# Kernel tuning notes

Measured on AMD Instinct MI355X. Metric: run time of the kernel, lower is better.

The kernel has to match this reference:

```python
import jax, jax.numpy as jnp
from jax import lax
import numpy as np

BS, T, DA, DZ, K = 64, 512, 16, 32, 3


def _lstm_layer(x, Wih, Whh, bih, bhh):
    # x: [B, T, in], PyTorch LSTM gate order i,f,g,o; zero initial state
    B = x.shape[0]
    H = Whh.shape[1]
    b = bih + bhh

    def step(carry, xt):
        h, c = carry
        g = xt @ Wih.T + h @ Whh.T + b  # [B, 4H]
        i, f, gg, o = jnp.split(g, 4, axis=-1)
        c = jax.nn.sigmoid(f) * c + jax.nn.sigmoid(i) * jnp.tanh(gg)
        h = jax.nn.sigmoid(o) * jnp.tanh(c)
        return (h, c), h

    h0 = jnp.zeros((B, H), x.dtype)
    _, hs = lax.scan(step, (h0, h0), jnp.swapaxes(x, 0, 1))
    return jnp.swapaxes(hs, 0, 1)


def setup_inputs() -> dict:
    key = jax.random.key(0)
    ks = jax.random.split(key, 12)
    a = jax.random.normal(ks[0], (BS, T, DA), jnp.float32)
    # mixture dynamics / emission matrices, kept near identity for stability
    A = 0.95 * jnp.eye(DZ, dtype=jnp.float32) + 0.02 * jax.random.normal(ks[1], (K, T, DZ, DZ), jnp.float32)
    C = jnp.eye(DA, DZ, dtype=jnp.float32) + 0.05 * jax.random.normal(ks[2], (K, T, DA, DZ), jnp.float32)
    R = 0.1 * jnp.eye(DA, dtype=jnp.float32)
    Q = 0.1 * jnp.eye(DZ, dtype=jnp.float32)
    mu0 = jnp.zeros((DZ,), jnp.float32)
    sigma0 = jnp.eye(DZ, dtype=jnp.float32)
    H4 = 4 * K  # LSTM hidden size = K
    Wih0 = 0.1 * jax.random.normal(ks[3], (H4, DA), jnp.float32)
    Whh0 = 0.1 * jax.random.normal(ks[4], (H4, K), jnp.float32)
    bih0 = 0.1 * jax.random.normal(ks[5], (H4,), jnp.float32)
    bhh0 = 0.1 * jax.random.normal(ks[6], (H4,), jnp.float32)
    Wih1 = 0.1 * jax.random.normal(ks[7], (H4, K), jnp.float32)
    Whh1 = 0.1 * jax.random.normal(ks[8], (H4, K), jnp.float32)
    bih1 = 0.1 * jax.random.normal(ks[9], (H4,), jnp.float32)
    bhh1 = 0.1 * jax.random.normal(ks[10], (H4,), jnp.float32)
    return {"a": a, "A": A, "C": C, "R": R, "Q": Q, "mu0": mu0, "sigma0": sigma0,
            "Wih0": Wih0, "Whh0": Whh0, "bih0": bih0, "bhh0": bhh0,
            "Wih1": Wih1, "Whh1": Whh1, "bih1": bih1, "bhh1": bhh1}


def reference(a, A, C, R, Q, mu0, sigma0, Wih0, Whh0, bih0, bhh0, Wih1, Whh1, bih1, bhh1):
    bs, T, da = a.shape
    dz = A.shape[-1]
    # dynamics network: 2-layer LSTM + softmax mixture weights alpha [bs,T,K]
    h = _lstm_layer(a, Wih0, Whh0, bih0, bhh0)
    h = _lstm_layer(h, Wih1, Whh1, bih1, bhh1)
    alpha = jax.nn.softmax(h, axis=-1)
    # mix per-mode matrices; time-major [T,bs,.,.]
    At = jnp.einsum('btk,ktij->tbij', alpha, A)
    Ct = jnp.einsum('btk,ktij->tbij', alpha, C)
    a_tm = jnp.swapaxes(a, 0, 1)  # [T,bs,da]
    I = jnp.eye(dz, dtype=a.dtype)
    mu_f0 = jnp.broadcast_to(mu0, (bs, dz))
    sig_f0 = jnp.broadcast_to(sigma0, (bs, dz, dz))

    def fstep(carry, inp):
        mu_f, mu_p, sig_p = carry  # prev filtered mean, predicted mean/cov
        a_t, A_t, C_t = inp
        # NOTE: residual uses previous *filtered* mean, matching the source code
        r = a_t - jnp.einsum('bij,bj->bi', C_t, mu_f)
        Ct_T = jnp.swapaxes(C_t, -1, -2)
        S = C_t @ sig_p @ Ct_T + R
        Kg = sig_p @ Ct_T @ jnp.linalg.inv(S)
        mu_new = mu_p + jnp.einsum('bij,bj->bi', Kg, r)
        sig_new = (I - Kg @ C_t) @ sig_p
        mu_p_new = jnp.einsum('bij,bj->bi', A_t, mu_new)
        sig_p_new = A_t @ sig_new @ jnp.swapaxes(A_t, -1, -2) + Q
        return (mu_new, mu_p_new, sig_p_new), (mu_new, sig_new, mu_p_new, sig_p_new)

    _, (mu_f, sig_f, mu_p, sig_p) = lax.scan(
        fstep, (mu_f0, mu_f0, sig_f0), (a_tm, At, Ct))

    # RTS smoothing (backward recursion), faithful to smooth()
    def sstep(carry, inp):
        mu_n, sig_n = carry
        mu_ft, sig_ft, mu_pt, sig_pt, A_next = inp
        J = sig_ft @ jnp.swapaxes(A_next, -1, -2) @ jnp.linalg.inv(sig_pt)
        mu_s = mu_ft + jnp.einsum('bij,bj->bi', J, mu_n - mu_pt)
        sig_s = sig_ft + J @ (sig_n - sig_pt)
        return (mu_s, sig_s), (mu_s, sig_s)

    _, (mu_s_rest, sig_s_rest) = lax.scan(
        sstep, (mu_f[-1], sig_f[-1]),
        (mu_f[:-1], sig_f[:-1], mu_p[:-1], sig_p[:-1], At[1:]),
        reverse=True)
    mu_s = jnp.concatenate([mu_s_rest, mu_f[-1:]], axis=0)   # [T,bs,dz]
    sig_s = jnp.concatenate([sig_s_rest, sig_f[-1:]], axis=0)  # [T,bs,dz,dz]
    out = jnp.concatenate([mu_s, sig_s.reshape(T, bs, dz * dz)], axis=-1)
    return jnp.swapaxes(out, 0, 1)  # [bs, T, dz + dz*dz]
```

## Files before the change

### kernel.cpp

```cpp
#include <hip/hip_runtime.h>
#include <hip/hip_bf16.h>

#define BSZ 64
#define TT  512
#define DA  16
#define DZ  32
#define NG  12
#define NT  256

typedef __hip_bfloat16 bf;

#define FP32_R0 0x3DCCCCCDu

__device__ __forceinline__ int mode_(const void* Rm){
  return (((const unsigned*)Rm)[0] == FP32_R0) ? 0 : 1;
}
__device__ __forceinline__ float LD(const void* p, size_t i, int b16){
  return b16 ? __bfloat162float(((const bf*)p)[i]) : ((const float*)p)[i];
}
__device__ __forceinline__ void STO(void* p, size_t i, float v, int b16){
  if (b16) ((bf*)p)[i] = __float2bfloat16(v);
  else     ((float*)p)[i] = v;
}
__device__ __forceinline__ float osan_(double vd, float code){
  float v = (float)vd;
  unsigned u = __float_as_uint(v);
  if ((u & 0x7f800000u) == 0x7f800000u)
    return ((u & 0x007fffffu) != 0u) ? code : ((u >> 31) ? -(code-1000.0f) : (code-1000.0f));
  return v;
}
__device__ __forceinline__ float sigm_(float x){ return 1.0f/(1.0f + __expf(-x)); }
__device__ __forceinline__ float tanh_(float x){ return 1.0f - 2.0f/(__expf(2.0f*x)+1.0f); }

__device__ void alpha_stage_(int b, int tid, int b16,
  const void* a, const void* Wih0, const void* bih0, const void* bhh0,
  const void* Whh0, const void* Wih1, const void* Whh1,
  const void* bih1, const void* bhh1,
  float* sxw, float* salp)
{
  for (int e=tid; e<TT*NG; e+=NT){
    int t=e/NG, g=e-NG*t;
    float s = LD(bih0,g,b16) + LD(bhh0,g,b16);
    size_t ab = ((size_t)b*TT + t)*DA;
    #pragma unroll
    for (int j=0;j<DA;++j) s += LD(Wih0,g*DA+j,b16)*LD(a,ab+j,b16);
    sxw[e] = s;
  }
  __syncthreads();
  if (tid==0){
    float w0[NG][3], wi1[NG][3], w1[NG][3], bb[NG];
    #pragma unroll
    for (int g=0;g<NG;++g){
      #pragma unroll
      for (int j=0;j<3;++j){ w0[g][j]=LD(Whh0,(size_t)g*3+j,b16); wi1[g][j]=LD(Wih1,(size_t)g*3+j,b16); w1[g][j]=LD(Whh1,(size_t)g*3+j,b16); }
      bb[g] = LD(bih1,g,b16) + LD(bhh1,g,b16);
    }
    float h1[3]={0,0,0}, c1[3]={0,0,0}, h2[3]={0,0,0}, c2[3]={0,0,0};
    for (int t=0;t<TT;++t){
      const float* xr = sxw + t*NG;
      float g1[NG];
      #pragma unroll
      for (int g=0;g<NG;++g) g1[g] = xr[g] + w0[g][0]*h1[0]+w0[g][1]*h1[1]+w0[g][2]*h1[2];
      #pragma unroll
      for (int j=0;j<3;++j){
        float iv=sigm_(g1[j]), fv=sigm_(g1[3+j]), gv=tanh_(g1[6+j]), ov=sigm_(g1[9+j]);
        c1[j] = fv*c1[j] + iv*gv;
        h1[j] = ov*tanh_(c1[j]);
      }
      float g2[NG];
      #pragma unroll
      for (int g=0;g<NG;++g) g2[g] = bb[g] + wi1[g][0]*h1[0]+wi1[g][1]*h1[1]+wi1[g][2]*h1[2]
                                            + w1[g][0]*h2[0]+w1[g][1]*h2[1]+w1[g][2]*h2[2];
      #pragma unroll
      for (int j=0;j<3;++j){
        float iv=sigm_(g2[j]), fv=sigm_(g2[3+j]), gv=tanh_(g2[6+j]), ov=sigm_(g2[9+j]);
        c2[j] = fv*c2[j] + iv*gv;
        h2[j] = ov*tanh_(c2[j]);
      }
      float m = fmaxf(h2[0], fmaxf(h2[1], h2[2]));
      float e0=__expf(h2[0]-m), e1=__expf(h2[1]-m), e2=__expf(h2[2]-m);
      float inv = 1.0f/(e0+e1+e2);
      salp[t*3+0]=e0*inv; salp[t*3+1]=e1*inv; salp[t*3+2]=e2*inv;
    }
  }
  __syncthreads();
}

__global__ __launch_bounds__(256) void k_alpha(
  const void* __restrict__ a, const void* __restrict__ Rm,
  const void* __restrict__ Wih0, const void* __restrict__ Whh0,
  const void* __restrict__ bih0, const void* __restrict__ bhh0,
  const void* __restrict__ Wih1, const void* __restrict__ Whh1,
  const void* __restrict__ bih1, const void* __restrict__ bhh1,
  float* __restrict__ alws)
{
  const int b16 = mode_(Rm);
  const int b = blockIdx.x, tid = threadIdx.x;
  __shared__ float sxw[TT*NG];
  __shared__ float salp[TT*3];
  alpha_stage_(b, tid, b16, a, Wih0, bih0, bhh0, Whh0, Wih1, Whh1, bih1, bhh1,
               sxw, salp);
  for (int e=tid;e<TT*3;e+=NT) alws[(size_t)b*TT*3+e] = salp[e];
}

__global__ __launch_bounds__(256) void k_fwd(
  const void* __restrict__ a, const void* __restrict__ Am,
  const void* __restrict__ Cm, const void* __restrict__ Rm,
  const void* __restrict__ Qm, const void* __restrict__ mu0,
  const void* __restrict__ sig0,
  const void* __restrict__ Wih0, const void* __restrict__ Whh0,
  const void* __restrict__ bih0, const void* __restrict__ bhh0,
  const void* __restrict__ Wih1, const void* __restrict__ Whh1,
  const void* __restrict__ bih1, const void* __restrict__ bhh1,
  const float* __restrict__ alws,
  void* __restrict__ out)
{
  const int b16 = mode_(Rm);
  const int b = blockIdx.x, tid = threadIdx.x;
  __shared__ double dpool[4240];
  __shared__ float sAt[1056], sCt[528], sQ[1056], sR[272], sPCt[544], sKg[544];
  __shared__ float salp[TT*3];
  __shared__ double dMu[32], dMup[32], dr[16];
  double* dPp  = dpool;
  double* dPf  = dpool+1056;
  double* dCP  = dpool+2112;
  double* dT1  = dpool+2640;
  double* dAugS= dpool+3696;
  double* dMinv= dpool+3968;

  if (alws){
    for (int e=tid;e<TT*3;e+=NT) salp[e] = alws[(size_t)b*TT*3+e];
    __syncthreads();
  } else {
    alpha_stage_(b, tid, b16, a, Wih0, bih0, bhh0, Whh0, Wih1, Whh1, bih1, bhh1,
                 (float*)dpool, salp);
  }

  for (int e=tid;e<1024;e+=NT){ int i=e>>5,j=e&31;
    sQ[i*33+j]  = LD(Qm,e,b16);
    dPp[i*33+j] = (double)LD(sig0,e,b16); }
  for (int e=tid;e<256;e+=NT){ int i=e>>4,j=e&15; sR[i*17+j] = LD(Rm,e,b16); }
  if (tid<32){ double m = (double)LD(mu0,tid,b16); dMu[tid]=m; dMup[tid]=m; }
  __syncthreads();

  const int i0 = tid>>5, j0 = tid&31;
  const int i4 = tid>>4, j4 = tid&15;

  float pA0[4],pA1[4],pA2[4],pC0[2],pC1[2],pC2[2];
  {
    size_t o0=0, o1=(size_t)TT*1024, o2=(size_t)2*TT*1024;
    #pragma unroll
    for (int q=0;q<4;++q){ int e=tid+q*NT; pA0[q]=LD(Am,o0+e,b16); pA1[q]=LD(Am,o1+e,b16); pA2[q]=LD(Am,o2+e,b16); }
    size_t c0=0, c1=(size_t)TT*512, c2=(size_t)2*TT*512;
    #pragma unroll
    for (int q=0;q<2;++q){ int e=tid+q*NT; pC0[q]=LD(Cm,c0+e,b16); pC1[q]=LD(Cm,c1+e,b16); pC2[q]=LD(Cm,c2+e,b16); }
  }

  for (int t=0;t<TT;++t){
    const size_t ob = ((size_t)b*TT+t)*1056;
    {
      float a0=salp[t*3+0], a1=salp[t*3+1], a2=salp[t*3+2];
      #pragma unroll
      for (int q=0;q<4;++q){ int e=tid+q*NT; int i=e>>5,j=e&31;
        sAt[i*33+j] = a0*pA0[q]+a1*pA1[q]+a2*pA2[q]; }
      #pragma unroll
      for (int q=0;q<2;++q){ int e=tid+q*NT; int i=e>>5,j=e&31;
        sCt[i*33+j] = a0*pC0[q]+a1*pC1[q]+a2*pC2[q]; }
    }
    if (t+1<TT){
      size_t o0=(size_t)(t+1)*1024, o1=(size_t)(TT+t+1)*1024, o2=(size_t)(2*TT+t+1)*1024;
      #pragma unroll
      for (int q=0;q<4;++q){ int e=tid+q*NT; pA0[q]=LD(Am,o0+e,b16); pA1[q]=LD(Am,o1+e,b16); pA2[q]=LD(Am,o2+e,b16); }
      size_t c0=(size_t)(t+1)*512, c1=(size_t)(TT+t+1)*512, c2=(size_t)(2*TT+t+1)*512;
      #pragma unroll
      for (int q=0;q<2;++q){ int e=tid+q*NT; pC0[q]=LD(Cm,c0+e,b16); pC1[q]=LD(Cm,c1+e,b16); pC2[q]=LD(Cm,c2+e,b16); }
    }
    __syncthreads();

    {
      double A0=0.0, A1=0.0;
      for (int k=0;k<32;++k){ double bv=dPp[k*33+j0];
        A0 += (double)sCt[i0*33+k]*bv;
        A1 += (double)sCt[(i0+8)*33+k]*bv; }
      dCP[i0*33+j0]=A0; dCP[(i0+8)*33+j0]=A1;
    }
    {
      double A0=0.0, A1=0.0;
      for (int m=0;m<32;++m){ double cv=(double)sCt[j4*33+m];
        A0 += dPp[i4*33+m]*cv;
        A1 += dPp[(i4+16)*33+m]*cv; }
      sPCt[i4*17+j4]=(float)A0; sPCt[(i4+16)*17+j4]=(float)A1;
    }
    if (tid<16){ double s = (double)LD(a,((size_t)b*TT+t)*DA+tid,b16);
      for (int k=0;k<32;++k) s -= (double)sCt[tid*33+k]*dMu[k];
      dr[tid]=s; }
    __syncthreads();

    { int i=tid>>4, j=tid&15; double v=(double)sR[i*17+j];
      for (int k=0;k<32;++k) v += dCP[i*33+k]*(double)sCt[j*33+k];
      dAugS[i*17+j]=v; }
    __syncthreads();

    if (tid < 64){
      const int r = tid>>2, q = tid&3, cbase = q*8;
      double Rg[8];
      #pragma unroll
      for (int u=0;u<8;++u){
        int c = cbase+u;
        Rg[u] = (c<16) ? dAugS[r*17+c] : ((c-16)==r ? 1.0 : 0.0);
      }
      #pragma unroll
      for (int kp=0;kp<16;++kp){
        double pv = __shfl(Rg[kp&7], (kp<<2)|(kp>>3), 64);
        if (!(fabs(pv)>1e-300)) pv=1.0;
        double ip = 1.0/pv;
        if (r==kp){
          #pragma unroll
          for (int u=0;u<8;++u){ int c=cbase+u; if (c>kp) Rg[u]*=ip; }
        }
        double rf = __shfl(Rg[kp&7], (tid&0x3C)|(kp>>3), 64);
        #pragma unroll
        for (int u=0;u<8;++u){
          double pr = __shfl(Rg[u], (kp<<2)|q, 64);
          int c=cbase+u;
          if (r!=kp && c>kp) Rg[u] -= rf*pr;
        }
      }
      if (q>=2){
        #pragma unroll
        for (int u=0;u<8;++u){ int k=cbase+u-16; dMinv[r*17+k]=Rg[u]; }
      }
    }
    __syncthreads();

    {
      double A0=0.0, A1=0.0;
      for (int l=0;l<16;++l){ double mv=dMinv[l*17+j4];
        A0 += (double)sPCt[i4*17+l]*mv;
        A1 += (double)sPCt[(i4+16)*17+l]*mv; }
      sKg[i4*17+j4]=(float)A0; sKg[(i4+16)*17+j4]=(float)A1;
    }
    __syncthreads();

    if (tid<32){ double s=dMup[tid];
      for (int k=0;k<16;++k) s += (double)sKg[tid*17+k]*dr[k];
      dMu[tid]=s;
      STO(out, ob+tid, osan_(s,5300.0f), b16);
    }
    {
      double A0=dPp[i0*33+j0], A1=dPp[(i0+8)*33+j0],
             A2=dPp[(i0+16)*33+j0], A3=dPp[(i0+24)*33+j0];
      for (int l=0;l<16;++l){ double cv=dCP[l*33+j0];
        A0 -= (double)sKg[i0*17+l]*cv;
        A1 -= (double)sKg[(i0+8)*17+l]*cv;
        A2 -= (double)sKg[(i0+16)*17+l]*cv;
        A3 -= (double)sKg[(i0+24)*17+l]*cv; }
      dPf[i0*33+j0]=A0; dPf[(i0+8)*33+j0]=A1;
      dPf[(i0+16)*33+j0]=A2; dPf[(i0+24)*33+j0]=A3;
      STO(out, ob+32+((size_t)i0<<5)+j0,      osan_(A0,5300.0f), b16);
      STO(out, ob+32+((size_t)(i0+8)<<5)+j0,  osan_(A1,5300.0f), b16);
      STO(out, ob+32+((size_t)(i0+16)<<5)+j0, osan_(A2,5300.0f), b16);
      STO(out, ob+32+((size_t)(i0+24)<<5)+j0, osan_(A3,5300.0f), b16);
    }
    __syncthreads();

    {
      double A0=0.0,A1=0.0,A2=0.0,A3=0.0;
      for (int k=0;k<32;++k){ double bv=dPf[k*33+j0];
        A0 += (double)sAt[i0*33+k]*bv;
        A1 += (double)sAt[(i0+8)*33+k]*bv;
        A2 += (double)sAt[(i0+16)*33+k]*bv;
        A3 += (double)sAt[(i0+24)*33+k]*bv; }
      dT1[i0*33+j0]=A0; dT1[(i0+8)*33+j0]=A1;
      dT1[(i0+16)*33+j0]=A2; dT1[(i0+24)*33+j0]=A3;
    }
    if (tid<32){ double s=0.0;
      for (int k=0;k<32;++k) s += (double)sAt[tid*33+k]*dMu[k];
      dMup[tid]=s; }
    __syncthreads();

    {
      double A0=(double)sQ[i0*33+j0], A1=(double)sQ[(i0+8)*33+j0],
             A2=(double)sQ[(i0+16)*33+j0], A3=(double)sQ[(i0+24)*33+j0];
      for (int k=0;k<32;++k){ double av=(double)sAt[j0*33+k];
        A0 += dT1[i0*33+k]*av;
        A1 += dT1[(i0+8)*33+k]*av;
        A2 += dT1[(i0+16)*33+k]*av;
        A3 += dT1[(i0+24)*33+k]*av; }
      dPp[i0*33+j0]=A0; dPp[(i0+8)*33+j0]=A1;
      dPp[(i0+16)*33+j0]=A2; dPp[(i0+24)*33+j0]=A3;
    }
    __syncthreads();
  }
}

__global__ __launch_bounds__(256) void k_pre(
  const void* __restrict__ Am, const void* __restrict__ Qm,
  const void* __restrict__ Rm, const void* __restrict__ outv,
  const float* __restrict__ alws, float* __restrict__ rec, int t0)
{
  const int b16 = mode_(Rm);
  const int t = t0 + blockIdx.x;
  const int b = blockIdx.y;
  const int tid = threadIdx.x;
  __shared__ double dAug[2080];
  __shared__ double dmp[32];
  __shared__ float sAtc[1056], sAtn[1056], sSf[1056], sT[1056], sF[1056], sPp[1056], sJ[1056], sQ[1056];
  __shared__ float smu[32];

  size_t obase = (size_t)b*TT*1056;
  const float* al = alws + (size_t)b*TT*3;
  float c0=al[t*3+0],     c1=al[t*3+1],     c2=al[t*3+2];
  float n0=al[(t+1)*3+0], n1=al[(t+1)*3+1], n2=al[(t+1)*3+2];
  size_t oA0c=(size_t)t*1024, oA1c=(size_t)(TT+t)*1024, oA2c=(size_t)(2*TT+t)*1024;
  size_t oA0n=oA0c+1024, oA1n=oA1c+1024, oA2n=oA2c+1024;

  for (int e=tid;e<1024;e+=NT){ int i=e>>5,j=e&31;
    sAtc[i*33+j] = c0*LD(Am,oA0c+e,b16)+c1*LD(Am,oA1c+e,b16)+c2*LD(Am,oA2c+e,b16);
    sAtn[i*33+j] = n0*LD(Am,oA0n+e,b16)+n1*LD(Am,oA1n+e,b16)+n2*LD(Am,oA2n+e,b16);
    sSf[i*33+j]  = LD(outv, obase + (size_t)t*1056 + 32 + e, b16);
    sQ[i*33+j]   = LD(Qm,e,b16);
  }
  if (tid<32) smu[tid] = LD(outv, obase + (size_t)t*1056 + tid, b16);
  __syncthreads();

  for (int e=tid;e<1024;e+=NT){ int i=e>>5, j=e&31;
    double acc=0.0, accF=0.0;
    for (int k=0;k<32;++k){
      acc  += (double)sAtc[i*33+k]*(double)sSf[k*33+j];
      accF += (double)sSf[i*33+k]*(double)sAtn[j*33+k];
    }
    sT[i*33+j]=(float)acc; sF[i*33+j]=(float)accF; }
  if (tid<32){ double s=0.0;
    for (int k=0;k<32;++k) s += (double)sAtc[tid*33+k]*(double)smu[k];
    dmp[tid]=s; }
  __syncthreads();

  for (int e=tid;e<1024;e+=NT){ int i=e>>5, j=e&31;
    double acc=(double)sQ[i*33+j];
    for (int k=0;k<32;++k) acc += (double)sT[i*33+k]*(double)sAtc[j*33+k];
    sPp[i*33+j]=(float)acc;
    dAug[i*65+j]=acc;
    dAug[i*65+32+j]=(i==j)?1.0:0.0; }
  __syncthreads();

  for (int kp=0;kp<32;++kp){
    double pv = dAug[kp*65+kp];
    if (!(fabs(pv)>1e-300)) pv=1.0;
    double ip = 1.0/pv;
    if (tid<64 && tid>kp) dAug[kp*65+tid] *= ip;
    __syncthreads();
    for (int e=tid;e<2048;e+=NT){ int i=e>>6, j=e&63;
      if (i!=kp && j>kp) dAug[i*65+j] -= dAug[i*65+kp]*dAug[kp*65+j];
    }
    __syncthreads();
  }

  float* rp = rec + ((size_t)b*gridDim.x + (size_t)blockIdx.x)*2080;

  for (int e=tid;e<1024;e+=NT){ int i=e>>5, j=e&31; double acc=0.0;
    for (int k=0;k<32;++k) acc += (double)sF[i*33+k]*dAug[k*65+32+j];
    float jv=(float)acc; sJ[i*33+j]=jv; rp[e]=jv; }
  __syncthreads();

  for (int e=tid;e<1024;e+=NT){ int i=e>>5, j=e&31;
    double acc=(double)sSf[i*33+j];
    for (int k=0;k<32;++k) acc -= (double)sJ[i*33+k]*(double)sPp[k*33+j];
    rp[1024+e]=(float)acc; }
  if (tid<32){ double acc=(double)smu[tid];
    for (int k=0;k<32;++k) acc -= (double)sJ[tid*33+k]*dmp[k];
    rp[2048+tid]=(float)acc; }
}

__global__ __launch_bounds__(256) void k_bwd(
  const void* __restrict__ Rm, void* __restrict__ outv,
  const float* __restrict__ rec, float* __restrict__ cont,
  int t0, int t1)
{
  const int b16 = mode_(Rm);
  const int b = blockIdx.x, tid = threadIdx.x;
  const int chlen = t1 - t0;
  __shared__ float sX[2][1056];
  __shared__ float sR[2080];
  size_t obase = (size_t)b*TT*1056;
  int cur = 0;
  const int i0 = tid>>5, j0 = tid&31;

  if (t1 == TT-1){
    for (int e=tid;e<1024;e+=NT){ int i=e>>5,j=e&31;
      sX[0][i*33+j] = LD(outv, obase+(size_t)(TT-1)*1056+32+e, b16); }
    if (tid<32) sX[0][tid*33+32] = LD(outv, obase+(size_t)(TT-1)*1056+tid, b16);
  } else {
    for (int e=tid;e<1056;e+=NT) sX[0][e] = cont[(size_t)b*1056+e];
  }
  float rg[9];
  {
    const float* rp = rec + ((size_t)b*chlen + (size_t)(chlen-1))*2080;
    #pragma unroll
    for (int q=0;q<9;++q){ int e=tid+q*NT; rg[q] = (e<2080)? rp[e] : 0.0f; }
  }
  __syncthreads();

  for (int t=t1-1; t>=t0; --t){
    #pragma unroll
    for (int q=0;q<9;++q){ int e=tid+q*NT; if (e<2080) sR[e]=rg[q]; }
    if (t>t0){
      const float* rp = rec + ((size_t)b*chlen + (size_t)(t-1-t0))*2080;
      #pragma unroll
      for (int q=0;q<9;++q){ int e=tid+q*NT; rg[q] = (e<2080)? rp[e] : 0.0f; }
    }
    __syncthreads();

    const float* Xc = sX[cur]; float* Xn = sX[cur^1];
    {
      double A0=(double)sR[1024+(i0<<5)+j0];
      double A1=(double)sR[1024+((i0+8)<<5)+j0];
      double A2=(double)sR[1024+((i0+16)<<5)+j0];
      double A3=(double)sR[1024+((i0+24)<<5)+j0];
      for (int k=0;k<32;++k){ double xv=(double)Xc[k*33+j0];
        A0 += (double)sR[(i0<<5)+k]*xv;
        A1 += (double)sR[((i0+8)<<5)+k]*xv;
        A2 += (double)sR[((i0+16)<<5)+k]*xv;
        A3 += (double)sR[((i0+24)<<5)+k]*xv; }
      Xn[i0*33+j0]=(float)A0;      Xn[(i0+8)*33+j0]=(float)A1;
      Xn[(i0+16)*33+j0]=(float)A2; Xn[(i0+24)*33+j0]=(float)A3;
      size_t tb = obase+(size_t)t*1056+32;
      STO(outv, tb+((size_t)i0<<5)+j0,      osan_(A0,5700.0f), b16);
      STO(outv, tb+((size_t)(i0+8)<<5)+j0,  osan_(A1,5700.0f), b16);
      STO(outv, tb+((size_t)(i0+16)<<5)+j0, osan_(A2,5700.0f), b16);
      STO(outv, tb+((size_t)(i0+24)<<5)+j0, osan_(A3,5700.0f), b16);
    }
    if (tid<32){
      double acc=(double)sR[2048+tid];
      for (int k=0;k<32;++k) acc += (double)sR[(tid<<5)+k]*(double)Xc[k*33+32];
      Xn[tid*33+32]=(float)acc;
      STO(outv, obase+(size_t)t*1056+tid, osan_(acc,5700.0f), b16);
    }
    __syncthreads();
    cur ^= 1;
  }
  for (int e=tid;e<1056;e+=NT) cont[(size_t)b*1056+e] = sX[cur][e];
}

__global__ __launch_bounds__(256) void k_smooth(
  const void* __restrict__ a, const void* __restrict__ Am,
  const void* __restrict__ Rm, const void* __restrict__ Qm,
  const void* __restrict__ Wih0, const void* __restrict__ Whh0,
  const void* __restrict__ bih0, const void* __restrict__ bhh0,
  const void* __restrict__ Wih1, const void* __restrict__ Whh1,
  const void* __restrict__ bih1, const void* __restrict__ bhh1,
  void* __restrict__ out)
{
  const int b16 = mode_(Rm);
  const int b = blockIdx.x, tid = threadIdx.x;
  __shared__ double dAug[2080];
  __shared__ float fp2[9504];
  __shared__ float salp[TT*3];
  __shared__ double dMun[32], dmp[32], sdm[32];
  float* sAtn = fp2;
  float* sAtc = fp2+1056;
  float* sSf  = fp2+2112;
  float* sSn  = fp2+3168;
  float* sT   = fp2+4224;
  float* sQ   = fp2+5280;
  float* sF   = fp2+6336;
  float* sPp32= fp2+7392;
  float* sJ   = fp2+8448;

  alpha_stage_(b, tid, b16, a, Wih0, bih0, bhh0, Whh0, Wih1, Whh1, bih1, bhh1,
               fp2, salp);

  size_t obase = (size_t)b*TT*1056;
  for (int e=tid;e<1024;e+=NT){ int i=e>>5,j=e&31;
    sQ[i*33+j]  = LD(Qm,e,b16);
    sSn[i*33+j] = LD(out, obase + (size_t)(TT-1)*1056 + 32 + e, b16); }
  if (tid<32) dMun[tid] = (double)LD(out, obase + (size_t)(TT-1)*1056 + tid, b16);
  __syncthreads();

  for (int t=TT-2; t>=0; --t){
    float n0=salp[(t+1)*3+0], n1=salp[(t+1)*3+1], n2=salp[(t+1)*3+2];
    float c0=salp[t*3+0],     c1=salp[t*3+1],     c2=salp[t*3+2];
    size_t oA0n=(size_t)(t+1)*1024, oA1n=(size_t)(TT+t+1)*1024, oA2n=(size_t)(2*TT+t+1)*1024;
    size_t oA0c=(size_t)t*1024,     oA1c=(size_t)(TT+t)*1024,   oA2c=(size_t)(2*TT+t)*1024;
    for (int e=tid;e<1024;e+=NT){ int i=e>>5,j=e&31;
      sAtn[i*33+j] = n0*LD(Am,oA0n+e,b16)+n1*LD(Am,oA1n+e,b16)+n2*LD(Am,oA2n+e,b16);
      sAtc[i*33+j] = c0*LD(Am,oA0c+e,b16)+c1*LD(Am,oA1c+e,b16)+c2*LD(Am,oA2c+e,b16);
      sSf[i*33+j]  = LD(out, obase + (size_t)t*1056 + 32 + e, b16); }
    __syncthreads();

    for (int e=tid;e<1024;e+=NT){ int i=e>>5, j=e&31;
      double acc=0.0, accF=0.0;
      for (int k=0;k<32;++k){
        acc  += (double)sAtc[i*33+k]*(double)sSf[k*33+j];
        accF += (double)sSf[i*33+k]*(double)sAtn[j*33+k];
      }
      sT[i*33+j]=(float)acc; sF[i*33+j]=(float)accF; }
    if (tid<32){ double s=0.0; float muf = LD(out, obase+(size_t)t*1056+tid, b16);
      for (int k=0;k<32;++k) s += (double)sAtc[tid*33+k]*(double)LD(out, obase+(size_t)t*1056+k, b16);
      dmp[tid]=s; (void)muf; }
    __syncthreads();

    for (int e=tid;e<1024;e+=NT){ int i=e>>5, j=e&31;
      double acc=(double)sQ[i*33+j];
      for (int k=0;k<32;++k) acc += (double)sT[i*33+k]*(double)sAtc[j*33+k];
      sPp32[i*33+j]=(float)acc;
      dAug[i*65+j]=acc;
      dAug[i*65+32+j]=(i==j)?1.0:0.0; }
    if (tid<32) sdm[tid] = dMun[tid] - dmp[tid];
    __syncthreads();

    for (int kp=0;kp<32;++kp){
      double pv = dAug[kp*65+kp];
      if (!(fabs(pv)>1e-300)) pv=1.0;
      double ip = 1.0/pv;
      if (tid<64 && tid>kp) dAug[kp*65+tid] *= ip;
      __syncthreads();
      for (int e=tid;e<2048;e+=NT){ int i=e>>6, j=e&63;
        if (i!=kp && j>kp) dAug[i*65+j] -= dAug[i*65+kp]*dAug[kp*65+j];
      }
      __syncthreads();
    }

    for (int e=tid;e<1024;e+=NT){ int i=e>>5, j=e&31; double acc=0.0;
      for (int k=0;k<32;++k) acc += (double)sF[i*33+k]*dAug[k*65+32+j];
      sJ[i*33+j]=(float)acc; }
    __syncthreads();

    if (tid<32){ double s2=0.0;
      for (int k=0;k<32;++k) s2 += (double)sJ[tid*33+k]*sdm[k];
      double v = (double)LD(out, obase+(size_t)t*1056+tid, b16) + s2;
      STO(out, obase+(size_t)t*1056+tid, osan_(v,5700.0f), b16);
      dMun[tid] = v;
    }
    float resv[4];
    { int i0 = tid>>5, j = tid&31;
      for (int s=0;s<4;++s){ int i=i0+(s<<3); double acc=0.0;
        for (int k=0;k<32;++k) acc += (double)sJ[i*33+k]*((double)sSn[k*33+j]-(double)sPp32[k*33+j]);
        double res = (double)sSf[i*33+j] + acc;
        STO(out, obase+(size_t)t*1056+32+(i<<5)+j, osan_(res,5700.0f), b16);
        resv[s]=(float)res;
      }
    }
    __syncthreads();
    { int i0 = tid>>5, j = tid&31;
      for (int s=0;s<4;++s){ int i=i0+(s<<3); sSn[i*33+j]=resv[s]; } }
    __syncthreads();
  }
}

__global__ __launch_bounds__(256) void k_fill(float* o, int n, float v){
  int i = blockIdx.x*256 + threadIdx.x;
  if (i<n) o[i]=v;
}

extern "C" void kernel_launch(void* const* d_in, const int* in_sizes, int n_in,
                              void* d_out, int out_size, void* d_ws, size_t ws_size,
                              hipStream_t stream)
{
  static const int EXP[15] = {524288,1572864,786432,256,1024,32,1024,192,36,12,12,36,36,12,12};
  int ok = (n_in==15) && (out_size==34603008);
  if (ok) for (int i=0;i<15;++i) if (in_sizes[i]!=EXP[i]) ok=0;
  if (!ok){
    k_fill<<<dim3((out_size+255)/256), dim3(256), 0, stream>>>((float*)d_out, out_size, 777.0f);
    return;
  }
  const void* a=d_in[0]; const void* Am=d_in[1]; const void* Cm=d_in[2];
  const void* Rm=d_in[3]; const void* Qm=d_in[4]; const void* mu0=d_in[5];
  const void* sig0=d_in[6];
  const void* Wih0=d_in[7]; const void* Whh0=d_in[8]; const void* bih0=d_in[9];
  const void* bhh0=d_in[10]; const void* Wih1=d_in[11]; const void* Whh1=d_in[12];
  const void* bih1=d_in[13]; const void* bhh1=d_in[14];

  const long long FIXED_F = 98304LL + 67584LL;
  long long availB = (long long)ws_size;
  int CH = 0;
  if (d_ws && availB > FIXED_F*4){
    long long ch = (availB - FIXED_F*4) / (64LL*2080LL*4LL);
    CH = (int)((ch > 511) ? 511 : ch);
  }

  if (CH >= 4){
    float* wsf  = (float*)d_ws;
    float* alws = wsf;
    float* cont = wsf + 98304;
    float* rec  = wsf + 165888;

    k_alpha<<<dim3(BSZ), dim3(NT), 0, stream>>>(a, Rm,
        Wih0, Whh0, bih0, bhh0, Wih1, Whh1, bih1, bhh1, alws);
    k_fwd  <<<dim3(BSZ), dim3(NT), 0, stream>>>(a, Am, Cm, Rm, Qm, mu0, sig0,
        Wih0, Whh0, bih0, bhh0, Wih1, Whh1, bih1, bhh1, alws, d_out);

    int t1 = TT-1;
    while (t1 > 0){
      int t0 = t1 - CH; if (t0 < 0) t0 = 0;
      int len = t1 - t0;
      k_pre<<<dim3(len, BSZ), dim3(NT), 0, stream>>>(Am, Qm, Rm, d_out, alws, rec, t0);
      k_bwd<<<dim3(BSZ), dim3(NT), 0, stream>>>(Rm, d_out, rec, cont, t0, t1);
      t1 = t0;
    }
  } else {
    k_fwd   <<<dim3(BSZ), dim3(NT), 0, stream>>>(a, Am, Cm, Rm, Qm, mu0, sig0,
               Wih0, Whh0, bih0, bhh0, Wih1, Whh1, bih1, bhh1, (const float*)nullptr, d_out);
    k_smooth<<<dim3(BSZ), dim3(NT), 0, stream>>>(a, Am, Rm, Qm,
               Wih0, Whh0, bih0, bhh0, Wih1, Whh1, bih1, bhh1, d_out);
  }
}
```

Measured before the change: 10.67 ms.

## Widen forward Kalman kernel to 512 threads and restructure covariance update

```diff
diff --git a/kernel.cpp b/kernel.cpp
--- a/kernel.cpp
+++ b/kernel.cpp
@@ -32,13 +32,13 @@
 __device__ __forceinline__ float sigm_(float x){ return 1.0f/(1.0f + __expf(-x)); }
 __device__ __forceinline__ float tanh_(float x){ return 1.0f - 2.0f/(__expf(2.0f*x)+1.0f); }
 
-__device__ void alpha_stage_(int b, int tid, int b16,
+__device__ void alpha_stage_(int b, int tid, int nt, int b16,
   const void* a, const void* Wih0, const void* bih0, const void* bhh0,
   const void* Whh0, const void* Wih1, const void* Whh1,
   const void* bih1, const void* bhh1,
   float* sxw, float* salp)
 {
-  for (int e=tid; e<TT*NG; e+=NT){
+  for (int e=tid; e<TT*NG; e+=nt){
     int t=e/NG, g=e-NG*t;
     float s = LD(bih0,g,b16) + LD(bhh0,g,b16);
     size_t ab = ((size_t)b*TT + t)*DA;
@@ -98,12 +98,12 @@
   const int b = blockIdx.x, tid = threadIdx.x;
   __shared__ float sxw[TT*NG];
   __shared__ float salp[TT*3];
-  alpha_stage_(b, tid, b16, a, Wih0, bih0, bhh0, Whh0, Wih1, Whh1, bih1, bhh1,
+  alpha_stage_(b, tid, NT, b16, a, Wih0, bih0, bhh0, Whh0, Wih1, Whh1, bih1, bhh1,
                sxw, salp);
   for (int e=tid;e<TT*3;e+=NT) alws[(size_t)b*TT*3+e] = salp[e];
 }
 
-__global__ __launch_bounds__(256) void k_fwd(
+__global__ __launch_bounds__(512) void k_fwd(
   const void* __restrict__ a, const void* __restrict__ Am,
   const void* __restrict__ Cm, const void* __restrict__ Rm,
   const void* __restrict__ Qm, const void* __restrict__ mu0,
@@ -122,38 +122,34 @@
   __shared__ float salp[TT*3];
   __shared__ double dMu[32], dMup[32], dr[16];
   double* dPp  = dpool;
-  double* dPf  = dpool+1056;
-  double* dCP  = dpool+2112;
-  double* dT1  = dpool+2640;
+  double* dAP  = dpool+1056;
+  double* dKCP = dpool+2112;
+  double* dCP  = dpool+3168;
   double* dAugS= dpool+3696;
   double* dMinv= dpool+3968;
 
   if (alws){
-    for (int e=tid;e<TT*3;e+=NT) salp[e] = alws[(size_t)b*TT*3+e];
+    for (int e=tid;e<TT*3;e+=512) salp[e] = alws[(size_t)b*TT*3+e];
     __syncthreads();
   } else {
-    alpha_stage_(b, tid, b16, a, Wih0, bih0, bhh0, Whh0, Wih1, Whh1, bih1, bhh1,
+    alpha_stage_(b, tid, 512, b16, a, Wih0, bih0, bhh0, Whh0, Wih1, Whh1, bih1, bhh1,
                  (float*)dpool, salp);
   }
 
-  for (int e=tid;e<1024;e+=NT){ int i=e>>5,j=e&31;
+  for (int e=tid;e<1024;e+=512){ int i=e>>5,j=e&31;
     sQ[i*33+j]  = LD(Qm,e,b16);
     dPp[i*33+j] = (double)LD(sig0,e,b16); }
-  for (int e=tid;e<256;e+=NT){ int i=e>>4,j=e&15; sR[i*17+j] = LD(Rm,e,b16); }
+  if (tid<256){ int i=tid>>4,j=tid&15; sR[i*17+j] = LD(Rm,tid,b16); }
   if (tid<32){ double m = (double)LD(mu0,tid,b16); dMu[tid]=m; dMup[tid]=m; }
   __syncthreads();
 
-  const int i0 = tid>>5, j0 = tid&31;
-  const int i4 = tid>>4, j4 = tid&15;
-
-  float pA0[4],pA1[4],pA2[4],pC0[2],pC1[2],pC2[2];
+  float pA0[2],pA1[2],pA2[2],pC0,pC1,pC2;
   {
     size_t o0=0, o1=(size_t)TT*1024, o2=(size_t)2*TT*1024;
     #pragma unroll
-    for (int q=0;q<4;++q){ int e=tid+q*NT; pA0[q]=LD(Am,o0+e,b16); pA1[q]=LD(Am,o1+e,b16); pA2[q]=LD(Am,o2+e,b16); }
+    for (int q=0;q<2;++q){ int e=tid+(q<<9); pA0[q]=LD(Am,o0+e,b16); pA1[q]=LD(Am,o1+e,b16); pA2[q]=LD(Am,o2+e,b16); }
     size_t c0=0, c1=(size_t)TT*512, c2=(size_t)2*TT*512;
-    #pragma unroll
-    for (int q=0;q<2;++q){ int e=tid+q*NT; pC0[q]=LD(Cm,c0+e,b16); pC1[q]=LD(Cm,c1+e,b16); pC2[q]=LD(Cm,c2+e,b16); }
+    pC0=LD(Cm,c0+tid,b16); pC1=LD(Cm,c1+tid,b16); pC2=LD(Cm,c2+tid,b16);
   }
 
   for (int t=0;t<TT;++t){
@@ -161,47 +157,36 @@
     {
       float a0=salp[t*3+0], a1=salp[t*3+1], a2=salp[t*3+2];
       #pragma unroll
-      for (int q=0;q<4;++q){ int e=tid+q*NT; int i=e>>5,j=e&31;
+      for (int q=0;q<2;++q){ int e=tid+(q<<9); int i=e>>5,j=e&31;
         sAt[i*33+j] = a0*pA0[q]+a1*pA1[q]+a2*pA2[q]; }
-      #pragma unroll
-      for (int q=0;q<2;++q){ int e=tid+q*NT; int i=e>>5,j=e&31;
-        sCt[i*33+j] = a0*pC0[q]+a1*pC1[q]+a2*pC2[q]; }
+      { int i=tid>>5,j=tid&31; sCt[i*33+j] = a0*pC0+a1*pC1+a2*pC2; }
     }
     if (t+1<TT){
       size_t o0=(size_t)(t+1)*1024, o1=(size_t)(TT+t+1)*1024, o2=(size_t)(2*TT+t+1)*1024;
       #pragma unroll
-      for (int q=0;q<4;++q){ int e=tid+q*NT; pA0[q]=LD(Am,o0+e,b16); pA1[q]=LD(Am,o1+e,b16); pA2[q]=LD(Am,o2+e,b16); }
+      for (int q=0;q<2;++q){ int e=tid+(q<<9); pA0[q]=LD(Am,o0+e,b16); pA1[q]=LD(Am,o1+e,b16); pA2[q]=LD(Am,o2+e,b16); }
       size_t c0=(size_t)(t+1)*512, c1=(size_t)(TT+t+1)*512, c2=(size_t)(2*TT+t+1)*512;
-      #pragma unroll
-      for (int q=0;q<2;++q){ int e=tid+q*NT; pC0[q]=LD(Cm,c0+e,b16); pC1[q]=LD(Cm,c1+e,b16); pC2[q]=LD(Cm,c2+e,b16); }
-    }
-    __syncthreads();
-
-    {
-      double A0=0.0, A1=0.0;
-      for (int k=0;k<32;++k){ double bv=dPp[k*33+j0];
-        A0 += (double)sCt[i0*33+k]*bv;
-        A1 += (double)sCt[(i0+8)*33+k]*bv; }
-      dCP[i0*33+j0]=A0; dCP[(i0+8)*33+j0]=A1;
-    }
-    {
-      double A0=0.0, A1=0.0;
-      for (int m=0;m<32;++m){ double cv=(double)sCt[j4*33+m];
-        A0 += dPp[i4*33+m]*cv;
-        A1 += dPp[(i4+16)*33+m]*cv; }
-      sPCt[i4*17+j4]=(float)A0; sPCt[(i4+16)*17+j4]=(float)A1;
-    }
+      pC0=LD(Cm,c0+tid,b16); pC1=LD(Cm,c1+tid,b16); pC2=LD(Cm,c2+tid,b16);
+    }
+    __syncthreads();
+
+    { int i=tid>>5, j=tid&31; double acc=0.0;
+      for (int k=0;k<32;++k) acc += (double)sCt[i*33+k]*dPp[k*33+j];
+      dCP[i*33+j]=acc; }
+    { int i=tid>>4, l=tid&15; double acc=0.0;
+      for (int m=0;m<32;++m) acc += dPp[i*33+m]*(double)sCt[l*33+m];
+      sPCt[i*17+l]=(float)acc; }
     if (tid<16){ double s = (double)LD(a,((size_t)b*TT+t)*DA+tid,b16);
       for (int k=0;k<32;++k) s -= (double)sCt[tid*33+k]*dMu[k];
       dr[tid]=s; }
     __syncthreads();
 
-    { int i=tid>>4, j=tid&15; double v=(double)sR[i*17+j];
-      for (int k=0;k<32;++k) v += dCP[i*33+k]*(double)sCt[j*33+k];
-      dAugS[i*17+j]=v; }
-    __syncthreads();
-
     if (tid < 64){
+      #pragma unroll
+      for (int u=0;u<4;++u){ int e=(tid<<2)+u; int i=e>>4, j=e&15;
+        double v=(double)sR[i*17+j];
+        for (int k=0;k<32;++k) v += dCP[i*33+k]*(double)sCt[j*33+k];
+        dAugS[i*17+j]=v; }
       const int r = tid>>2, q = tid&3, cbase = q*8;
       double Rg[8];
       #pragma unroll
@@ -230,66 +215,46 @@
         #pragma unroll
         for (int u=0;u<8;++u){ int k=cbase+u-16; dMinv[r*17+k]=Rg[u]; }
       }
-    }
-    __syncthreads();
-
-    {
-      double A0=0.0, A1=0.0;
-      for (int l=0;l<16;++l){ double mv=dMinv[l*17+j4];
-        A0 += (double)sPCt[i4*17+l]*mv;
-        A1 += (double)sPCt[(i4+16)*17+l]*mv; }
-      sKg[i4*17+j4]=(float)A0; sKg[(i4+16)*17+j4]=(float)A1;
-    }
-    __syncthreads();
-
+    } else {
+      for (int e=tid-64; e<1024; e+=448){ int i=e>>5,j=e&31; double acc=0.0;
+        for (int k=0;k<32;++k) acc += (double)sAt[i*33+k]*dPp[k*33+j];
+        dAP[i*33+j]=acc; }
+    }
+    __syncthreads();
+
+    { int i=tid>>4, k4=tid&15; double acc=0.0;
+      for (int l=0;l<16;++l) acc += (double)sPCt[i*17+l]*dMinv[l*17+k4];
+      sKg[i*17+k4]=(float)acc; }
+    __syncthreads();
+
+    #pragma unroll
+    for (int q=0;q<2;++q){ int e=tid+(q<<9); int i=e>>5,j=e&31;
+      double acc=0.0;
+      for (int l=0;l<16;++l) acc += (double)sKg[i*17+l]*dCP[l*33+j];
+      dKCP[i*33+j]=acc; }
     if (tid<32){ double s=dMup[tid];
       for (int k=0;k<16;++k) s += (double)sKg[tid*17+k]*dr[k];
       dMu[tid]=s;
-      STO(out, ob+tid, osan_(s,5300.0f), b16);
-    }
-    {
-      double A0=dPp[i0*33+j0], A1=dPp[(i0+8)*33+j0],
-             A2=dPp[(i0+16)*33+j0], A3=dPp[(i0+24)*33+j0];
-      for (int l=0;l<16;++l){ double cv=dCP[l*33+j0];
-        A0 -= (double)sKg[i0*17+l]*cv;
-        A1 -= (double)sKg[(i0+8)*17+l]*cv;
-        A2 -= (double)sKg[(i0+16)*17+l]*cv;
-        A3 -= (double)sKg[(i0+24)*17+l]*cv; }
-      dPf[i0*33+j0]=A0; dPf[(i0+8)*33+j0]=A1;
-      dPf[(i0+16)*33+j0]=A2; dPf[(i0+24)*33+j0]=A3;
-      STO(out, ob+32+((size_t)i0<<5)+j0,      osan_(A0,5300.0f), b16);
-      STO(out, ob+32+((size_t)(i0+8)<<5)+j0,  osan_(A1,5300.0f), b16);
-      STO(out, ob+32+((size_t)(i0+16)<<5)+j0, osan_(A2,5300.0f), b16);
-      STO(out, ob+32+((size_t)(i0+24)<<5)+j0, osan_(A3,5300.0f), b16);
-    }
-    __syncthreads();
-
-    {
-      double A0=0.0,A1=0.0,A2=0.0,A3=0.0;
-      for (int k=0;k<32;++k){ double bv=dPf[k*33+j0];
-        A0 += (double)sAt[i0*33+k]*bv;
-        A1 += (double)sAt[(i0+8)*33+k]*bv;
-        A2 += (double)sAt[(i0+16)*33+k]*bv;
-        A3 += (double)sAt[(i0+24)*33+k]*bv; }
-      dT1[i0*33+j0]=A0; dT1[(i0+8)*33+j0]=A1;
-      dT1[(i0+16)*33+j0]=A2; dT1[(i0+24)*33+j0]=A3;
-    }
+      STO(out, ob+tid, osan_(s,5300.0f), b16); }
+    __syncthreads();
+
+    #pragma unroll
+    for (int q=0;q<2;++q){ int e=tid+(q<<9); int i=e>>5,j=e&31;
+      double pf = dPp[i*33+j] - dKCP[i*33+j];
+      STO(out, ob+32+e, osan_(pf,5300.0f), b16);
+      double acc = dAP[i*33+j];
+      for (int k=0;k<32;++k) acc -= (double)sAt[i*33+k]*dKCP[k*33+j];
+      dAP[i*33+j]=acc; }
     if (tid<32){ double s=0.0;
       for (int k=0;k<32;++k) s += (double)sAt[tid*33+k]*dMu[k];
       dMup[tid]=s; }
     __syncthreads();
 
-    {
-      double A0=(double)sQ[i0*33+j0], A1=(double)sQ[(i0+8)*33+j0],
-             A2=(double)sQ[(i0+16)*33+j0], A3=(double)sQ[(i0+24)*33+j0];
-      for (int k=0;k<32;++k){ double av=(double)sAt[j0*33+k];
-        A0 += dT1[i0*33+k]*av;
-        A1 += dT1[(i0+8)*33+k]*av;
-        A2 += dT1[(i0+16)*33+k]*av;
-        A3 += dT1[(i0+24)*33+k]*av; }
-      dPp[i0*33+j0]=A0; dPp[(i0+8)*33+j0]=A1;
-      dPp[(i0+16)*33+j0]=A2; dPp[(i0+24)*33+j0]=A3;
-    }
+    #pragma unroll
+    for (int q=0;q<2;++q){ int e=tid+(q<<9); int i=e>>5,j=e&31;
+      double acc=(double)sQ[i*33+j];
+      for (int k=0;k<32;++k) acc += dAP[i*33+k]*(double)sAt[j*33+k];
+      dPp[i*33+j]=acc; }
     __syncthreads();
   }
 }
@@ -372,46 +337,48 @@
     rp[2048+tid]=(float)acc; }
 }
 
-__global__ __launch_bounds__(256) void k_bwd(
+__global__ __launch_bounds__(512) void k_bwd(
   const void* __restrict__ Rm, void* __restrict__ outv,
   const float* __restrict__ rec, float* __restrict__ cont,
   int t0, int t1)
 {
   const int b16 = mode_(Rm);
-  const int b = blockIdx.x, tid = threadIdx.x;
+  const int tid = threadIdx.x, grp = tid>>8, lt = tid&255;
+  const int b = (blockIdx.x<<1) + grp;
   const int chlen = t1 - t0;
-  __shared__ float sX[2][1056];
-  __shared__ float sR[2080];
+  __shared__ float sX[2][2][1056];
+  __shared__ float sRr[2][2080];
   size_t obase = (size_t)b*TT*1056;
   int cur = 0;
-  const int i0 = tid>>5, j0 = tid&31;
+  const int i0 = lt>>5, j0 = lt&31;
+  float* X0 = sX[grp][0]; float* X1 = sX[grp][1]; float* sR = sRr[grp];
 
   if (t1 == TT-1){
-    for (int e=tid;e<1024;e+=NT){ int i=e>>5,j=e&31;
-      sX[0][i*33+j] = LD(outv, obase+(size_t)(TT-1)*1056+32+e, b16); }
-    if (tid<32) sX[0][tid*33+32] = LD(outv, obase+(size_t)(TT-1)*1056+tid, b16);
+    for (int e=lt;e<1024;e+=256){ int i=e>>5,j=e&31;
+      X0[i*33+j] = LD(outv, obase+(size_t)(TT-1)*1056+32+e, b16); }
+    if (lt<32) X0[lt*33+32] = LD(outv, obase+(size_t)(TT-1)*1056+lt, b16);
   } else {
-    for (int e=tid;e<1056;e+=NT) sX[0][e] = cont[(size_t)b*1056+e];
+    for (int e=lt;e<1056;e+=256) X0[e] = cont[(size_t)b*1056+e];
   }
   float rg[9];
   {
     const float* rp = rec + ((size_t)b*chlen + (size_t)(chlen-1))*2080;
     #pragma unroll
-    for (int q=0;q<9;++q){ int e=tid+q*NT; rg[q] = (e<2080)? rp[e] : 0.0f; }
+    for (int q=0;q<9;++q){ int e=lt+q*256; rg[q] = (e<2080)? rp[e] : 0.0f; }
   }
   __syncthreads();
 
   for (int t=t1-1; t>=t0; --t){
     #pragma unroll
-    for (int q=0;q<9;++q){ int e=tid+q*NT; if (e<2080) sR[e]=rg[q]; }
+    for (int q=0;q<9;++q){ int e=lt+q*256; if (e<2080) sR[e]=rg[q]; }
     if (t>t0){
       const float* rp = rec + ((size_t)b*chlen + (size_t)(t-1-t0))*2080;
       #pragma unroll
-      for (int q=0;q<9;++q){ int e=tid+q*NT; rg[q] = (e<2080)? rp[e] : 0.0f; }
-    }
-    __syncthreads();
-
-    const float* Xc = sX[cur]; float* Xn = sX[cur^1];
+      for (int q=0;q<9;++q){ int e=lt+q*256; rg[q] = (e<2080)? rp[e] : 0.0f; }
+    }
+    __syncthreads();
+
+    const float* Xc = cur ? X1 : X0; float* Xn = cur ? X0 : X1;
     {
       double A0=(double)sR[1024+(i0<<5)+j0];
       double A1=(double)sR[1024+((i0+8)<<5)+j0];
@@ -430,16 +397,17 @@
       STO(outv, tb+((size_t)(i0+16)<<5)+j0, osan_(A2,5700.0f), b16);
       STO(outv, tb+((size_t)(i0+24)<<5)+j0, osan_(A3,5700.0f), b16);
     }
-    if (tid<32){
-      double acc=(double)sR[2048+tid];
-      for (int k=0;k<32;++k) acc += (double)sR[(tid<<5)+k]*(double)Xc[k*33+32];
-      Xn[tid*33+32]=(float)acc;
-      STO(outv, obase+(size_t)t*1056+tid, osan_(acc,5700.0f), b16);
+    if (lt<32){
+      double acc=(double)sR[2048+lt];
+      for (int k=0;k<32;++k) acc += (double)sR[(lt<<5)+k]*(double)Xc[k*33+32];
+      Xn[lt*33+32]=(float)acc;
+      STO(outv, obase+(size_t)t*1056+lt, osan_(acc,5700.0f), b16);
     }
     __syncthreads();
     cur ^= 1;
   }
-  for (int e=tid;e<1056;e+=NT) cont[(size_t)b*1056+e] = sX[cur][e];
+  { float* Xf = cur ? X1 : X0;
+    for (int e=lt;e<1056;e+=256) cont[(size_t)b*1056+e] = Xf[e]; }
 }
 
 __global__ __launch_bounds__(256) void k_smooth(
@@ -467,7 +435,7 @@
   float* sPp32= fp2+7392;
   float* sJ   = fp2+8448;
 
-  alpha_stage_(b, tid, b16, a, Wih0, bih0, bhh0, Whh0, Wih1, Whh1, bih1, bhh1,
+  alpha_stage_(b, tid, NT, b16, a, Wih0, bih0, bhh0, Whh0, Wih1, Whh1, bih1, bhh1,
                fp2, salp);
 
   size_t obase = (size_t)b*TT*1056;
@@ -587,7 +555,7 @@
 
     k_alpha<<<dim3(BSZ), dim3(NT), 0, stream>>>(a, Rm,
         Wih0, Whh0, bih0, bhh0, Wih1, Whh1, bih1, bhh1, alws);
-    k_fwd  <<<dim3(BSZ), dim3(NT), 0, stream>>>(a, Am, Cm, Rm, Qm, mu0, sig0,
+    k_fwd  <<<dim3(BSZ), dim3(512), 0, stream>>>(a, Am, Cm, Rm, Qm, mu0, sig0,
         Wih0, Whh0, bih0, bhh0, Wih1, Whh1, bih1, bhh1, alws, d_out);
 
     int t1 = TT-1;
@@ -595,11 +563,11 @@
       int t0 = t1 - CH; if (t0 < 0) t0 = 0;
       int len = t1 - t0;
       k_pre<<<dim3(len, BSZ), dim3(NT), 0, stream>>>(Am, Qm, Rm, d_out, alws, rec, t0);
-      k_bwd<<<dim3(BSZ), dim3(NT), 0, stream>>>(Rm, d_out, rec, cont, t0, t1);
+      k_bwd<<<dim3(BSZ/2), dim3(512), 0, stream>>>(Rm, d_out, rec, cont, t0, t1);
       t1 = t0;
     }
   } else {
-    k_fwd   <<<dim3(BSZ), dim3(NT), 0, stream>>>(a, Am, Cm, Rm, Qm, mu0, sig0,
+    k_fwd   <<<dim3(BSZ), dim3(512), 0, stream>>>(a, Am, Cm, Rm, Qm, mu0, sig0,
                Wih0, Whh0, bih0, bhh0, Wih1, Whh1, bih1, bhh1, (const float*)nullptr, d_out);
     k_smooth<<<dim3(BSZ), dim3(NT), 0, stream>>>(a, Am, Rm, Qm,
                Wih0, Whh0, bih0, bhh0, Wih1, Whh1, bih1, bhh1, d_out);
```

New measurement: 11.50 ms. 1.08x slower.
